# Performance work log

Measured on AMD Instinct MI355X. Metric: run time of the kernel, lower is better.

Reference implementation:

```python
import jax, jax.numpy as jnp
import numpy as np

B, N, D, H = 2, 2048, 384, 8
Dh = D // H          # 48
G = Dh // 3          # 16 3-vectors per head
EPS = 1e-5


def setup_inputs() -> dict:
    key = jax.random.key(0)
    ks = jax.random.split(key, 8)
    x = jax.random.normal(ks[0], (B, N, D), dtype=jnp.float32)
    # per-node SE(3) frames: proper rotation matrices via QR of random Gaussians
    raw = jax.random.normal(ks[1], (B, N, 3, 3), dtype=jnp.float32)
    q, r = jnp.linalg.qr(raw)
    sign = jnp.sign(jnp.diagonal(r, axis1=-2, axis2=-1))
    frames = q * sign[..., None, :]
    s = 1.0 / np.sqrt(D)
    Wq = jax.random.normal(ks[2], (D, D), dtype=jnp.float32) * s
    Wk = jax.random.normal(ks[3], (D, D), dtype=jnp.float32) * s
    Wv = jax.random.normal(ks[4], (D, D), dtype=jnp.float32) * s
    Wo = jax.random.normal(ks[5], (D, D), dtype=jnp.float32) * s
    bo = jnp.zeros((D,), dtype=jnp.float32)
    gamma = jnp.ones((D,), dtype=jnp.float32)
    beta = jnp.zeros((D,), dtype=jnp.float32)
    return {"x": x, "frames": frames, "Wq": Wq, "Wk": Wk, "Wv": Wv,
            "Wo": Wo, "bo": bo, "gamma": gamma, "beta": beta}


def _rotate(frames, t):
    # t: [B,N,H,Dh] -> rotate each 3-vector chunk by the node's frame R_i
    b, n, h, dh = t.shape
    t3 = t.reshape(b, n, h, dh // 3, 3)
    r3 = jnp.einsum('bnij,bnhgj->bnhgi', frames, t3)
    return r3.reshape(b, n, h, dh)


def reference(x, frames, Wq, Wk, Wv, Wo, bo, gamma, beta):
    b, n, d = x.shape
    Q = (x @ Wq.T).reshape(b, n, H, Dh)
    K = (x @ Wk.T).reshape(b, n, H, Dh)
    V = (x @ Wv.T).reshape(b, n, H, Dh)
    # SE(3) frame-conditioned attention: rotate Q,K into each node's local frame
    Qr = _rotate(frames, Q)
    Kr = _rotate(frames, K)
    scores = jnp.einsum('bqhd,bkhd->bhqk', Qr, Kr) / np.sqrt(Dh)
    attn = jax.nn.softmax(scores, axis=-1)
    out = jnp.einsum('bhqk,bkhd->bqhd', attn, V).reshape(b, n, d)
    out = out @ Wo.T + bo          # out_proj; dropout is identity in eval
    y = x + out                     # residual
    mu = jnp.mean(y, axis=-1, keepdims=True)
    var = jnp.var(y, axis=-1, keepdims=True)
    return (y - mu) * jax.lax.rsqrt(var + EPS) * gamma + beta
```

## Files before the change

kernel.cpp:

```cpp
#include <hip/hip_runtime.h>
#include <hip/hip_bf16.h>
#include <math.h>

constexpr int B = 2, N = 2048, D = 384, H = 8, Dh = 48;
constexpr int M = B * N;
constexpr float EPS = 1e-5f;
constexpr int WSZ = 384 * 384;

typedef short bf16x8 __attribute__((ext_vector_type(8)));
typedef float f32x4 __attribute__((ext_vector_type(4)));

#if __has_builtin(__builtin_amdgcn_exp2f)
#define EXP2(x) __builtin_amdgcn_exp2f(x)
#else
#define EXP2(x) exp2f(x)
#endif

__device__ __forceinline__ ushort f2bf(float f) {
  union { float f; uint u; } v; v.f = f;
  uint r = v.u + 0x7fffu + ((v.u >> 16) & 1u);
  return (ushort)(r >> 16);
}
__device__ __forceinline__ float bf2f(ushort u) {
  union { uint u; float f; } v; v.u = ((uint)u) << 16;
  return v.f;
}
__device__ __forceinline__ uint pk_bf16(float lo, float hi) {
  union { __hip_bfloat162 h; uint u; } v;
  v.h = __float22bfloat162_rn(make_float2(lo, hi));
  return v.u;
}

__device__ __forceinline__ void gload16(const void* g, void* lds) {
  __builtin_amdgcn_global_load_lds(
      (const __attribute__((address_space(1))) unsigned int*)g,
      (__attribute__((address_space(3))) unsigned int*)lds, 16, 0, 0);
}

__global__ __launch_bounds__(256) void pack_all(
    const float* __restrict__ x, const float* __restrict__ Wq,
    const float* __restrict__ Wk, const float* __restrict__ Wv,
    const float* __restrict__ Wo, ushort* __restrict__ xbf,
    ushort* __restrict__ Wqkv, ushort* __restrict__ Wobf) {
  constexpr int XSZ = M * 384;
  int i = (blockIdx.x * 256 + threadIdx.x) * 8;
  const float* src; ushort* dst; int off;
  if (i < XSZ) { src = x; dst = xbf; off = i; }
  else {
    int j = i - XSZ;
    if (j < WSZ)          { src = Wq; dst = Wqkv;           off = j; }
    else if (j < 2 * WSZ) { src = Wk; dst = Wqkv + WSZ;     off = j - WSZ; }
    else if (j < 3 * WSZ) { src = Wv; dst = Wqkv + 2 * WSZ; off = j - 2 * WSZ; }
    else                  { src = Wo; dst = Wobf;           off = j - 3 * WSZ; }
  }
  float4 a = *(const float4*)(src + off);
  float4 b = *(const float4*)(src + off + 4);
  uint4 o;
  o.x = pk_bf16(a.x, a.y);
  o.y = pk_bf16(a.z, a.w);
  o.z = pk_bf16(b.x, b.y);
  o.w = pk_bf16(b.z, b.w);
  *(uint4*)(dst + off) = o;
}

__global__ __launch_bounds__(256) void gemm_qkv(
    const ushort* __restrict__ Abf, const ushort* __restrict__ Wbf,
    ushort* __restrict__ Qpad, ushort* __restrict__ Kpad,
    ushort* __restrict__ Vt) {
  __shared__ ushort Asm[64 * 32];
  __shared__ ushort Bsm[128 * 32];
  const int tid = threadIdx.x, w = tid >> 6, lane = tid & 63;
  const int lq = lane & 15, g = lane >> 4;
  const int brow = blockIdx.y * 64, bcol = blockIdx.x * 128;
  const int wr0 = (w >> 1) * 32, wc0 = (w & 1) * 64;
  const int srow = lane >> 2, scol = (lane & 3) * 8;
  f32x4 acc[2][4];
#pragma unroll
  for (int mi = 0; mi < 2; ++mi)
#pragma unroll
    for (int ni = 0; ni < 4; ++ni) acc[mi][ni] = f32x4{0.f, 0.f, 0.f, 0.f};

  for (int kt = 0; kt < 384; kt += 32) {
    __syncthreads();
    gload16(Abf + (size_t)(brow + w * 16 + srow) * 384 + kt + scol, Asm + w * 512);
#pragma unroll
    for (int i = 0; i < 2; ++i) {
      int seg = w * 2 + i;
      gload16(Wbf + (size_t)(bcol + seg * 16 + srow) * 384 + kt + scol, Bsm + seg * 512);
    }
    __syncthreads();
    bf16x8 a[2], b[4];
#pragma unroll
    for (int mi = 0; mi < 2; ++mi)
      a[mi] = *(const bf16x8*)(Asm + (wr0 + mi * 16 + lq) * 32 + g * 8);
#pragma unroll
    for (int ni = 0; ni < 4; ++ni)
      b[ni] = *(const bf16x8*)(Bsm + (wc0 + ni * 16 + lq) * 32 + g * 8);
#pragma unroll
    for (int mi = 0; mi < 2; ++mi)
#pragma unroll
      for (int ni = 0; ni < 4; ++ni)
        acc[mi][ni] = __builtin_amdgcn_mfma_f32_16x16x32_bf16(a[mi], b[ni], acc[mi][ni], 0, 0, 0);
  }

  if (bcol < 768) {
#pragma unroll
    for (int mi = 0; mi < 2; ++mi)
#pragma unroll
      for (int ni = 0; ni < 4; ++ni) {
        int colD = bcol + wc0 + ni * 16 + lq;
        ushort* dstm = (colD < 384) ? Qpad : Kpad;
        int c = (colD < 384) ? colD : colD - 384;
        int hh = c / 48, dh = c - hh * 48;
#pragma unroll
        for (int r = 0; r < 4; ++r) {
          int row = brow + wr0 + mi * 16 + g * 4 + r;
          dstm[(size_t)row * 512 + hh * 64 + dh] = f2bf(acc[mi][ni][r]);
        }
      }
  } else {
#pragma unroll
    for (int mi = 0; mi < 2; ++mi)
#pragma unroll
      for (int ni = 0; ni < 4; ++ni) {
        int vcol = bcol + wc0 + ni * 16 + lq - 768;
        int hh = vcol / 48, dh = vcol - hh * 48;
#pragma unroll
        for (int r = 0; r < 4; ++r) {
          int row = brow + wr0 + mi * 16 + g * 4 + r;
          int bb = row >> 11, nn = row & 2047;
          Vt[((size_t)(bb * H + hh) * 48 + dh) * N + nn] = f2bf(acc[mi][ni][r]);
        }
      }
  }
}

__global__ __launch_bounds__(256) void rotate_both(
    ushort* __restrict__ Q, ushort* __restrict__ K,
    const float* __restrict__ F, float qscale) {
  int idx = blockIdx.x * 256 + threadIdx.x;
  int h = idx & 7;
  int bn = (idx >> 3) & 4095;
  int mat = idx >> 15;
  ushort* p = (mat ? K : Q) + (size_t)bn * 512 + h * 64;
  float scale = mat ? 1.0f : qscale;
  const float* R = F + (size_t)bn * 9;
  float r0 = R[0], r1 = R[1], r2 = R[2];
  float r3 = R[3], r4 = R[4], r5 = R[5];
  float r6 = R[6], r7 = R[7], r8 = R[8];
  uint u[24];
#pragma unroll
  for (int j = 0; j < 6; ++j)
    *(uint4*)(u + j * 4) = *(const uint4*)(p + j * 8);
  float f[48];
#pragma unroll
  for (int j = 0; j < 24; ++j) {
    f[2 * j] = bf2f((ushort)u[j]);
    f[2 * j + 1] = bf2f((ushort)(u[j] >> 16));
  }
  float o[48];
#pragma unroll
  for (int t = 0; t < 16; ++t) {
    float v0 = f[3 * t], v1 = f[3 * t + 1], v2 = f[3 * t + 2];
    o[3 * t]     = (r0 * v0 + r1 * v1 + r2 * v2) * scale;
    o[3 * t + 1] = (r3 * v0 + r4 * v1 + r5 * v2) * scale;
    o[3 * t + 2] = (r6 * v0 + r7 * v1 + r8 * v2) * scale;
  }
  uint ow[24];
#pragma unroll
  for (int j = 0; j < 24; ++j) ow[j] = pk_bf16(o[2 * j], o[2 * j + 1]);
#pragma unroll
  for (int j = 0; j < 6; ++j)
    *(uint4*)(p + j * 8) = *(uint4*)(ow + j * 4);
  uint4 z = make_uint4(0, 0, 0, 0);
  *(uint4*)(p + 48) = z;
  *(uint4*)(p + 56) = z;
}

__global__ __launch_bounds__(256) void attn_mfma(
    const ushort* __restrict__ Qpad, const ushort* __restrict__ Kpad,
    const ushort* __restrict__ Vt, ushort* __restrict__ Pacc,
    float* __restrict__ Pml) {
  __shared__ __align__(16) ushort SH[8192];
  ushort* K0 = SH;
  ushort* K1 = SH + 4096;

  const int bid = blockIdx.x;
  const int wg = (bid & 7) * 64 + (bid >> 3);
  const int qt = wg & 15;
  const int rest = wg >> 4;
  const int h = rest & 7;
  const int b = (rest >> 3) & 1;
  const int half = rest >> 4;
  const int kt0 = half * 1024;
  const int tid = threadIdx.x;
  const int w = tid >> 6;
  const int lane = tid & 63;
  const int lq = lane & 15;
  const int g = lane >> 4;
  const int l7 = lq & 7;
  const int srow8 = lane >> 3;
  const int c8 = (lane & 7) ^ srow8;

  bf16x8 qf[2][2];
  {
    const ushort* qb = Qpad + ((size_t)(b * N) + qt * 128 + w * 32) * 512 + h * 64;
#pragma unroll
    for (int i = 0; i < 2; ++i)
#pragma unroll
      for (int kd = 0; kd < 2; ++kd)
        qf[i][kd] = *(const bf16x8*)(qb + (size_t)(i * 16 + lq) * 512 + kd * 32 + g * 8);
  }

  const ushort* kg0;
  const ushort* kg1;
  {
    int s0 = w;
    int k0i = (s0 >> 2) * 32 + (s0 & 1) * 16 + (srow8 >> 2) * 8 + ((s0 >> 1) & 1) * 4 + (srow8 & 3);
    kg0 = Kpad + ((size_t)(b * N) + kt0 + k0i) * 512 + h * 64 + c8 * 8;
    int s1 = w + 4;
    int k1i = (s1 >> 2) * 32 + (s1 & 1) * 16 + (srow8 >> 2) * 8 + ((s1 >> 1) & 1) * 4 + (srow8 & 3);
    kg1 = Kpad + ((size_t)(b * N) + kt0 + k1i) * 512 + h * 64 + c8 * 8;
  }
  const ushort* vbase = Vt + ((size_t)(b * H + h) * 48 + lq) * (size_t)N + kt0 + g * 8;

  auto stage = [&](ushort* kb) {
    gload16(kg0, kb + w * 512);
    gload16(kg1, kb + (w + 4) * 512);
    kg0 += 64 * 512; kg1 += 64 * 512;
  };

  float m[2] = {-3.0e38f, -3.0e38f}, l[2] = {0.f, 0.f};
  f32x4 oacc[2][3];
#pragma unroll
  for (int i = 0; i < 2; ++i)
#pragma unroll
    for (int d = 0; d < 3; ++d) oacc[i][d] = f32x4{0.f, 0.f, 0.f, 0.f};

  stage(K0);
  __syncthreads();
  int cur = 0;

  for (int t = 0; t < 16; ++t) {
    if (t < 15) stage(cur ? K0 : K1);
    const ushort* Kc = cur ? K1 : K0;

    bf16x8 vf[2][3];
#pragma unroll
    for (int ks = 0; ks < 2; ++ks)
#pragma unroll
      for (int d = 0; d < 3; ++d)
        vf[ks][d] = *(const bf16x8*)(vbase + (size_t)(d * 16) * N + ks * 32);

    f32x4 st[2][4];
#pragma unroll
    for (int i = 0; i < 2; ++i)
#pragma unroll
      for (int t4 = 0; t4 < 4; ++t4) st[i][t4] = f32x4{0.f, 0.f, 0.f, 0.f};
#pragma unroll
    for (int t4 = 0; t4 < 4; ++t4) {
      bf16x8 a0 = *(const bf16x8*)(Kc + (t4 * 16 + lq) * 64 + ((g ^ l7) * 8));
      bf16x8 a1 = *(const bf16x8*)(Kc + (t4 * 16 + lq) * 64 + (((g + 4) ^ l7) * 8));
#pragma unroll
      for (int i = 0; i < 2; ++i) {
        st[i][t4] = __builtin_amdgcn_mfma_f32_16x16x32_bf16(a0, qf[i][0], st[i][t4], 0, 0, 0);
        st[i][t4] = __builtin_amdgcn_mfma_f32_16x16x32_bf16(a1, qf[i][1], st[i][t4], 0, 0, 0);
      }
    }

    float tmax[2];
#pragma unroll
    for (int i = 0; i < 2; ++i) {
      float t0 = st[i][0][0];
#pragma unroll
      for (int t4 = 0; t4 < 4; ++t4)
#pragma unroll
        for (int r = 0; r < 4; ++r) t0 = fmaxf(t0, st[i][t4][r]);
      t0 = fmaxf(t0, __shfl_xor(t0, 16));
      t0 = fmaxf(t0, __shfl_xor(t0, 32));
      tmax[i] = t0;
    }
    bool need = (tmax[0] > m[0] + 8.0f) | (tmax[1] > m[1] + 8.0f);
    if (__ballot(need)) {
#pragma unroll
      for (int i = 0; i < 2; ++i) {
        float mnew = fmaxf(m[i], tmax[i]);
        float corr = EXP2(m[i] - mnew);
        m[i] = mnew;
        l[i] *= corr;
#pragma unroll
        for (int r = 0; r < 4; ++r) {
          float cr = __shfl(corr, g * 4 + r);
#pragma unroll
          for (int d = 0; d < 3; ++d) oacc[i][d][r] *= cr;
        }
      }
    }

    bf16x8 pf[2][2];
#pragma unroll
    for (int i = 0; i < 2; ++i) {
      float ps = 0.f;
      uint u0[4], u1[4];
#pragma unroll
      for (int t4 = 0; t4 < 4; ++t4) {
        float p0 = EXP2(st[i][t4][0] - m[i]);
        float p1 = EXP2(st[i][t4][1] - m[i]);
        float p2 = EXP2(st[i][t4][2] - m[i]);
        float p3 = EXP2(st[i][t4][3] - m[i]);
        ps += (p0 + p1) + (p2 + p3);
        if (t4 < 2) {
          u0[(t4 & 1) * 2]     = pk_bf16(p0, p1);
          u0[(t4 & 1) * 2 + 1] = pk_bf16(p2, p3);
        } else {
          u1[(t4 & 1) * 2]     = pk_bf16(p0, p1);
          u1[(t4 & 1) * 2 + 1] = pk_bf16(p2, p3);
        }
      }
      ps += __shfl_xor(ps, 16);
      ps += __shfl_xor(ps, 32);
      l[i] += ps;
      union { uint4 q; bf16x8 v; } c0, c1;
      c0.q = make_uint4(u0[0], u0[1], u0[2], u0[3]);
      c1.q = make_uint4(u1[0], u1[1], u1[2], u1[3]);
      pf[i][0] = c0.v;
      pf[i][1] = c1.v;
    }

#pragma unroll
    for (int ks = 0; ks < 2; ++ks)
#pragma unroll
      for (int i = 0; i < 2; ++i)
#pragma unroll
        for (int d = 0; d < 3; ++d)
          oacc[i][d] = __builtin_amdgcn_mfma_f32_16x16x32_bf16(pf[i][ks], vf[ks][d], oacc[i][d], 0, 0, 0);

    vbase += 64;
    __syncthreads();
    cur ^= 1;
  }

#pragma unroll
  for (int i = 0; i < 2; ++i) {
    const size_t pr0 = ((size_t)((half * B + b) * H + h)) * N + qt * 128 + w * 32 + i * 16;
#pragma unroll
    for (int d = 0; d < 3; ++d)
#pragma unroll
      for (int r = 0; r < 4; ++r)
        Pacc[(pr0 + g * 4 + r) * 48 + d * 16 + lq] = f2bf(oacc[i][d][r]);
    if (g == 0) {
      Pml[(pr0 + lq) * 2] = m[i];
      Pml[(pr0 + lq) * 2 + 1] = l[i];
    }
  }
}

__global__ __launch_bounds__(256) void gemm_out_ln(
    const ushort* __restrict__ Pacc, const float* __restrict__ Pml,
    const ushort* __restrict__ Wbf, const float* __restrict__ x,
    const float* __restrict__ bo, const float* __restrict__ gamma,
    const float* __restrict__ beta, float* __restrict__ out) {
  __shared__ ushort Asm[16 * 32];
  __shared__ ushort Bsm[384 * 32];
  __shared__ float red[4][16][2];
  __shared__ float Wm[16][8][2];
  const int tid = threadIdx.x, w = tid >> 6, lane = tid & 63;
  const int lq = lane & 15, g = lane >> 4;
  const int brow = blockIdx.x * 16;
  const int srow = lane >> 2, scol = (lane & 3) * 8;

  if (tid < 128) {
    int r = tid >> 3, hh = tid & 7;
    int gr = brow + r;
    int bb = gr >> 11, nn = gr & 2047;
    size_t i0 = ((size_t)(bb * H + hh)) * N + nn;
    size_t i1 = ((size_t)((B + bb) * H + hh)) * N + nn;
    float m0 = Pml[i0 * 2], l0 = Pml[i0 * 2 + 1];
    float m1 = Pml[i1 * 2], l1 = Pml[i1 * 2 + 1];
    float mm = fmaxf(m0, m1);
    float e0 = EXP2(m0 - mm), e1 = EXP2(m1 - mm);
    float inv = 1.f / (l0 * e0 + l1 * e1);
    Wm[r][hh][0] = e0 * inv;
    Wm[r][hh][1] = e1 * inv;
  }
  __syncthreads();

  f32x4 acc[6];
#pragma unroll
  for (int ni = 0; ni < 6; ++ni) acc[ni] = f32x4{0.f, 0.f, 0.f, 0.f};

  for (int kt = 0; kt < 384; kt += 32) {
    __syncthreads();
    if (w == 0) {
      int col = kt + scol;
      int hh = col / 48;
      int dcol = col - hh * 48;
      int gr = brow + srow;
      int bb = gr >> 11, nn = gr & 2047;
      const ushort* a0p = Pacc + (((size_t)(bb * H + hh)) * N + nn) * 48 + dcol;
      const ushort* a1p = Pacc + (((size_t)((B + bb) * H + hh)) * N + nn) * 48 + dcol;
      bf16x8 a0 = *(const bf16x8*)a0p;
      bf16x8 a1 = *(const bf16x8*)a1p;
      float w0v = Wm[srow][hh][0], w1v = Wm[srow][hh][1];
      uint mg[4];
#pragma unroll
      for (int j = 0; j < 4; ++j)
        mg[j] = pk_bf16(
            bf2f((ushort)a0[2 * j]) * w0v + bf2f((ushort)a1[2 * j]) * w1v,
            bf2f((ushort)a0[2 * j + 1]) * w0v + bf2f((ushort)a1[2 * j + 1]) * w1v);
      *(uint4*)(Asm + srow * 32 + scol) = make_uint4(mg[0], mg[1], mg[2], mg[3]);
    }
#pragma unroll
    for (int i = 0; i < 6; ++i) {
      int seg = w * 6 + i;
      gload16(Wbf + (size_t)(seg * 16 + srow) * 384 + kt + scol, Bsm + seg * 512);
    }
    __syncthreads();
    bf16x8 a = *(const bf16x8*)(Asm + lq * 32 + g * 8);
#pragma unroll
    for (int ni = 0; ni < 6; ++ni) {
      bf16x8 bb2 = *(const bf16x8*)(Bsm + ((w * 6 + ni) * 16 + lq) * 32 + g * 8);
      acc[ni] = __builtin_amdgcn_mfma_f32_16x16x32_bf16(a, bb2, acc[ni], 0, 0, 0);
    }
  }

  float s[4] = {0.f, 0.f, 0.f, 0.f}, s2[4] = {0.f, 0.f, 0.f, 0.f};
#pragma unroll
  for (int ni = 0; ni < 6; ++ni) {
    int col = (w * 6 + ni) * 16 + lq;
    float bcol = bo[col];
#pragma unroll
    for (int r = 0; r < 4; ++r) {
      float y = acc[ni][r] + x[(size_t)(brow + g * 4 + r) * 384 + col] + bcol;
      acc[ni][r] = y;
      s[r] += y; s2[r] += y * y;
    }
  }
#pragma unroll
  for (int o = 1; o < 16; o <<= 1) {
#pragma unroll
    for (int r = 0; r < 4; ++r) {
      s[r] += __shfl_xor(s[r], o);
      s2[r] += __shfl_xor(s2[r], o);
    }
  }
  if (lq == 0) {
#pragma unroll
    for (int r = 0; r < 4; ++r) {
      red[w][g * 4 + r][0] = s[r];
      red[w][g * 4 + r][1] = s2[r];
    }
  }
  __syncthreads();
#pragma unroll
  for (int r = 0; r < 4; ++r) {
    int row = g * 4 + r;
    float ts  = red[0][row][0] + red[1][row][0] + red[2][row][0] + red[3][row][0];
    float ts2 = red[0][row][1] + red[1][row][1] + red[2][row][1] + red[3][row][1];
    float mu = ts * (1.f / 384.f);
    float var = ts2 * (1.f / 384.f) - mu * mu;
    float rstd = rsqrtf(var + EPS);
    float* orow = out + (size_t)(brow + row) * 384;
#pragma unroll
    for (int ni = 0; ni < 6; ++ni) {
      int col = (w * 6 + ni) * 16 + lq;
      orow[col] = (acc[ni][r] - mu) * rstd * gamma[col] + beta[col];
    }
  }
}

extern "C" void kernel_launch(void* const* d_in, const int* in_sizes, int n_in,
                              void* d_out, int out_size, void* d_ws, size_t ws_size,
                              hipStream_t stream) {
  const float* x      = (const float*)d_in[0];
  const float* frames = (const float*)d_in[1];
  const float* Wq     = (const float*)d_in[2];
  const float* Wk     = (const float*)d_in[3];
  const float* Wv     = (const float*)d_in[4];
  const float* Wo     = (const float*)d_in[5];
  const float* bo     = (const float*)d_in[6];
  const float* gamma  = (const float*)d_in[7];
  const float* beta   = (const float*)d_in[8];
  float* out = (float*)d_out;

  ushort* xbf  = (ushort*)d_ws;
  ushort* Wqkv = xbf + (size_t)M * 384;
  ushort* Wobf = Wqkv + 3 * (size_t)WSZ;
  ushort* Qpad = Wobf + (size_t)WSZ;
  ushort* Kpad = Qpad + (size_t)M * 512;
  ushort* Vt   = Kpad + (size_t)M * 512;
  ushort* Pacc = Vt + (size_t)M * 384;
  float*  Pml  = (float*)(Pacc + (size_t)2 * B * H * N * 48);

  const float qscale = 0.14433756729740643f * 1.4426950408889634f;

  pack_all<<<(M * 384 + 4 * WSZ) / (8 * 256), 256, 0, stream>>>(
      x, Wq, Wk, Wv, Wo, xbf, Wqkv, Wobf);

  gemm_qkv<<<dim3(9, 64), 256, 0, stream>>>(xbf, Wqkv, Qpad, Kpad, Vt);

  rotate_both<<<2 * M * H / 256, 256, 0, stream>>>(Qpad, Kpad, frames, qscale);

  attn_mfma<<<2 * B * H * (N / 128), 256, 0, stream>>>(Qpad, Kpad, Vt, Pacc, Pml);

  gemm_out_ln<<<M / 16, 256, 0, stream>>>(Pacc, Pml, Wobf, x, bo, gamma, beta, out);
}
```

Measured before the change: 75.65 us.

## Fuse frame rotation and Q scaling into QKV GEMM epilogue via LDS staging

Removes the separate rotate_both kernel by staging each Q/K GEMM tile in shared memory and applying the per-node frame rotation and Q scale in the epilogue, with coalesced 16-byte writes to the padded Q/K buffers. The GEMM tile changes from 64x128 to 128x96 so one column tile covers exactly two heads, giving a 12x32 grid. This saves a kernel launch and a full read/write round trip of Q and K, at the cost of an extra LDS pass, extra syncs and fewer blocks (384 vs 576).

Measured after the change: 74.07 us. 1.02x faster.

```diff
diff --git a/kernel.cpp b/kernel.cpp
--- a/kernel.cpp
+++ b/kernel.cpp
@@ -65,65 +65,55 @@
 
 __global__ __launch_bounds__(256) void gemm_qkv(
     const ushort* __restrict__ Abf, const ushort* __restrict__ Wbf,
-    ushort* __restrict__ Qpad, ushort* __restrict__ Kpad,
-    ushort* __restrict__ Vt) {
-  __shared__ ushort Asm[64 * 32];
-  __shared__ ushort Bsm[128 * 32];
+    const float* __restrict__ F, ushort* __restrict__ Qpad,
+    ushort* __restrict__ Kpad, ushort* __restrict__ Vt, float qscale) {
+  __shared__ __align__(16) ushort SH[128 * 96];
+  ushort* Asm = SH;
+  ushort* Bsm = SH + 4096;
   const int tid = threadIdx.x, w = tid >> 6, lane = tid & 63;
   const int lq = lane & 15, g = lane >> 4;
-  const int brow = blockIdx.y * 64, bcol = blockIdx.x * 128;
-  const int wr0 = (w >> 1) * 32, wc0 = (w & 1) * 64;
+  const int brow = blockIdx.y * 128;
+  const int bx = blockIdx.x;
+  const int bcol = bx * 96;
+  const int wr0 = (w >> 1) * 64, wc0 = (w & 1) * 48;
   const int srow = lane >> 2, scol = (lane & 3) * 8;
-  f32x4 acc[2][4];
-#pragma unroll
-  for (int mi = 0; mi < 2; ++mi)
-#pragma unroll
-    for (int ni = 0; ni < 4; ++ni) acc[mi][ni] = f32x4{0.f, 0.f, 0.f, 0.f};
+
+  f32x4 acc[4][3];
+#pragma unroll
+  for (int mi = 0; mi < 4; ++mi)
+#pragma unroll
+    for (int ni = 0; ni < 3; ++ni) acc[mi][ni] = f32x4{0.f, 0.f, 0.f, 0.f};
 
   for (int kt = 0; kt < 384; kt += 32) {
     __syncthreads();
-    gload16(Abf + (size_t)(brow + w * 16 + srow) * 384 + kt + scol, Asm + w * 512);
-#pragma unroll
-    for (int i = 0; i < 2; ++i) {
-      int seg = w * 2 + i;
-      gload16(Wbf + (size_t)(bcol + seg * 16 + srow) * 384 + kt + scol, Bsm + seg * 512);
+    for (int s = w; s < 14; s += 4) {
+      if (s < 8)
+        gload16(Abf + (size_t)(brow + s * 16 + srow) * 384 + kt + scol, Asm + s * 512);
+      else
+        gload16(Wbf + (size_t)(bcol + (s - 8) * 16 + srow) * 384 + kt + scol,
+                Bsm + (s - 8) * 512);
     }
     __syncthreads();
-    bf16x8 a[2], b[4];
-#pragma unroll
-    for (int mi = 0; mi < 2; ++mi)
+    bf16x8 a[4], b[3];
+#pragma unroll
+    for (int mi = 0; mi < 4; ++mi)
       a[mi] = *(const bf16x8*)(Asm + (wr0 + mi * 16 + lq) * 32 + g * 8);
 #pragma unroll
-    for (int ni = 0; ni < 4; ++ni)
+    for (int ni = 0; ni < 3; ++ni)
       b[ni] = *(const bf16x8*)(Bsm + (wc0 + ni * 16 + lq) * 32 + g * 8);
 #pragma unroll
-    for (int mi = 0; mi < 2; ++mi)
-#pragma unroll
-      for (int ni = 0; ni < 4; ++ni)
+    for (int mi = 0; mi < 4; ++mi)
+#pragma unroll
+      for (int ni = 0; ni < 3; ++ni)
         acc[mi][ni] = __builtin_amdgcn_mfma_f32_16x16x32_bf16(a[mi], b[ni], acc[mi][ni], 0, 0, 0);
   }
 
-  if (bcol < 768) {
-#pragma unroll
-    for (int mi = 0; mi < 2; ++mi)
-#pragma unroll
-      for (int ni = 0; ni < 4; ++ni) {
-        int colD = bcol + wc0 + ni * 16 + lq;
-        ushort* dstm = (colD < 384) ? Qpad : Kpad;
-        int c = (colD < 384) ? colD : colD - 384;
-        int hh = c / 48, dh = c - hh * 48;
-#pragma unroll
-        for (int r = 0; r < 4; ++r) {
-          int row = brow + wr0 + mi * 16 + g * 4 + r;
-          dstm[(size_t)row * 512 + hh * 64 + dh] = f2bf(acc[mi][ni][r]);
-        }
-      }
-  } else {
-#pragma unroll
-    for (int mi = 0; mi < 2; ++mi)
-#pragma unroll
-      for (int ni = 0; ni < 4; ++ni) {
-        int vcol = bcol + wc0 + ni * 16 + lq - 768;
+  if (bx >= 8) {
+#pragma unroll
+    for (int mi = 0; mi < 4; ++mi)
+#pragma unroll
+      for (int ni = 0; ni < 3; ++ni) {
+        int vcol = (bx - 8) * 96 + wc0 + ni * 16 + lq;
         int hh = vcol / 48, dh = vcol - hh * 48;
 #pragma unroll
         for (int r = 0; r < 4; ++r) {
@@ -132,49 +122,68 @@
           Vt[((size_t)(bb * H + hh) * 48 + dh) * N + nn] = f2bf(acc[mi][ni][r]);
         }
       }
-  }
-}
-
-__global__ __launch_bounds__(256) void rotate_both(
-    ushort* __restrict__ Q, ushort* __restrict__ K,
-    const float* __restrict__ F, float qscale) {
-  int idx = blockIdx.x * 256 + threadIdx.x;
-  int h = idx & 7;
-  int bn = (idx >> 3) & 4095;
-  int mat = idx >> 15;
-  ushort* p = (mat ? K : Q) + (size_t)bn * 512 + h * 64;
-  float scale = mat ? 1.0f : qscale;
-  const float* R = F + (size_t)bn * 9;
-  float r0 = R[0], r1 = R[1], r2 = R[2];
-  float r3 = R[3], r4 = R[4], r5 = R[5];
-  float r6 = R[6], r7 = R[7], r8 = R[8];
-  uint u[24];
-#pragma unroll
-  for (int j = 0; j < 6; ++j)
-    *(uint4*)(u + j * 4) = *(const uint4*)(p + j * 8);
-  float f[48];
-#pragma unroll
-  for (int j = 0; j < 24; ++j) {
-    f[2 * j] = bf2f((ushort)u[j]);
-    f[2 * j + 1] = bf2f((ushort)(u[j] >> 16));
-  }
-  float o[48];
-#pragma unroll
-  for (int t = 0; t < 16; ++t) {
-    float v0 = f[3 * t], v1 = f[3 * t + 1], v2 = f[3 * t + 2];
-    o[3 * t]     = (r0 * v0 + r1 * v1 + r2 * v2) * scale;
-    o[3 * t + 1] = (r3 * v0 + r4 * v1 + r5 * v2) * scale;
-    o[3 * t + 2] = (r6 * v0 + r7 * v1 + r8 * v2) * scale;
-  }
-  uint ow[24];
-#pragma unroll
-  for (int j = 0; j < 24; ++j) ow[j] = pk_bf16(o[2 * j], o[2 * j + 1]);
-#pragma unroll
-  for (int j = 0; j < 6; ++j)
-    *(uint4*)(p + j * 8) = *(uint4*)(ow + j * 4);
-  uint4 z = make_uint4(0, 0, 0, 0);
-  *(uint4*)(p + 48) = z;
-  *(uint4*)(p + 56) = z;
+    return;
+  }
+
+  __syncthreads();
+#pragma unroll
+  for (int mi = 0; mi < 4; ++mi)
+#pragma unroll
+    for (int ni = 0; ni < 3; ++ni) {
+      int col = wc0 + ni * 16 + lq;
+#pragma unroll
+      for (int r = 0; r < 4; ++r)
+        SH[(wr0 + mi * 16 + g * 4 + r) * 96 + col] = f2bf(acc[mi][ni][r]);
+    }
+  __syncthreads();
+
+  ushort* dstm = (bx < 4) ? Qpad : Kpad;
+  const int hb = (bx & 3) * 2;
+  const float scale = (bx < 4) ? qscale : 1.0f;
+#pragma unroll
+  for (int it = 0; it < 2; ++it) {
+    int task = tid + it * 256;
+    int row = task >> 2;
+    int hh = (task >> 1) & 1;
+    int half = task & 1;
+    int bn = brow + row;
+    const float* R = F + (size_t)bn * 9;
+    float r0 = R[0], r1 = R[1], r2 = R[2];
+    float r3 = R[3], r4 = R[4], r5 = R[5];
+    float r6 = R[6], r7 = R[7], r8 = R[8];
+    const ushort* src = SH + row * 96 + hh * 48 + half * 24;
+    uint u[12];
+    *(uint4*)(u)     = *(const uint4*)(src);
+    *(uint4*)(u + 4) = *(const uint4*)(src + 8);
+    *(uint4*)(u + 8) = *(const uint4*)(src + 16);
+    float f[24];
+#pragma unroll
+    for (int j = 0; j < 12; ++j) {
+      f[2 * j] = bf2f((ushort)u[j]);
+      f[2 * j + 1] = bf2f((ushort)(u[j] >> 16));
+    }
+    float o[24];
+#pragma unroll
+    for (int t = 0; t < 8; ++t) {
+      float v0 = f[3 * t], v1 = f[3 * t + 1], v2 = f[3 * t + 2];
+      o[3 * t]     = (r0 * v0 + r1 * v1 + r2 * v2) * scale;
+      o[3 * t + 1] = (r3 * v0 + r4 * v1 + r5 * v2) * scale;
+      o[3 * t + 2] = (r6 * v0 + r7 * v1 + r8 * v2) * scale;
+    }
+    uint ow[12];
+#pragma unroll
+    for (int j = 0; j < 12; ++j) ow[j] = pk_bf16(o[2 * j], o[2 * j + 1]);
+    ushort* dp = dstm + (size_t)bn * 512 + (hb + hh) * 64 + half * 24;
+    *(uint4*)(dp)      = *(uint4*)(ow);
+    *(uint4*)(dp + 8)  = *(uint4*)(ow + 4);
+    *(uint4*)(dp + 16) = *(uint4*)(ow + 8);
+    if (half) {
+      uint4 z = make_uint4(0, 0, 0, 0);
+      ushort* zp = dstm + (size_t)bn * 512 + (hb + hh) * 64 + 48;
+      *(uint4*)(zp) = z;
+      *(uint4*)(zp + 8) = z;
+    }
+  }
 }
 
 __global__ __launch_bounds__(256) void attn_mfma(
@@ -497,9 +506,7 @@
   pack_all<<<(M * 384 + 4 * WSZ) / (8 * 256), 256, 0, stream>>>(
       x, Wq, Wk, Wv, Wo, xbf, Wqkv, Wobf);
 
-  gemm_qkv<<<dim3(9, 64), 256, 0, stream>>>(xbf, Wqkv, Qpad, Kpad, Vt);
-
-  rotate_both<<<2 * M * H / 256, 256, 0, stream>>>(Qpad, Kpad, frames, qscale);
+  gemm_qkv<<<dim3(12, 32), 256, 0, stream>>>(xbf, Wqkv, frames, Qpad, Kpad, Vt, qscale);
 
   attn_mfma<<<2 * B * H * (N / 128), 256, 0, stream>>>(Qpad, Kpad, Vt, Pacc, Pml);
 
```
